# Kernel optimization log

Hardware: AMD Instinct MI355X
Metric: run time of the kernel (lower is better)

## Reference

```python
import jax, jax.numpy as jnp
import numpy as np

KSIZE = 7       # patch size
STRIDE_Q = 4    # stride_1: query patch stride
STRIDE_KV = 1   # stride_2: key/value patch stride
SCALE = 10.0    # softmax_scale


def unfold(x, k, stride, pad):
    """torch.nn.Unfold equivalent. x:[B,C,H,W] -> [B, C*k*k, L] (c-major, then kh, kw)."""
    x = jnp.pad(x, ((0, 0), (0, 0), (pad, pad), (pad, pad)))
    B, C, Hp, Wp = x.shape
    nh = (Hp - k) // stride + 1
    nw = (Wp - k) // stride + 1
    sl = lambda i, n: slice(i, i + (n - 1) * stride + 1, stride)
    # [B, C, k*k, nh, nw]
    pat = jnp.stack([x[:, :, sl(i, nh), sl(j, nw)] for i in range(k) for j in range(k)], axis=2)
    return pat.reshape(B, C * k * k, nh * nw)


def fold(p, k, stride, pad, H, W):
    """torch.nn.functional.fold equivalent (overlap-add). p:[B, C*k*k, L] -> [B,C,H,W]."""
    B, D, L = p.shape
    C = D // (k * k)
    nh = (H + 2 * pad - k) // stride + 1
    nw = (W + 2 * pad - k) // stride + 1
    p = p.reshape(B, C, k, k, nh, nw)
    out = jnp.zeros((B, C, H + 2 * pad, W + 2 * pad), p.dtype)
    sl = lambda i, n: slice(i, i + (n - 1) * stride + 1, stride)
    for i in range(k):
        for j in range(k):
            out = out.at[:, :, sl(i, nh), sl(j, nw)].add(p[:, :, i, j])
    return out[:, :, pad:pad + H, pad:pad + W]


def conv1x1(x, w, bias):
    # w: [out, in]
    return jnp.einsum('bihw,oi->bohw', x, w) + bias[None, :, None, None]


def setup_inputs() -> dict:
    key = jax.random.key(0)
    ks = jax.random.split(key, 9)
    B, Cin, H, W = 4, 64, 128, 128
    Cit = 16
    s_in = 1.0 / np.sqrt(Cin)
    s_it = 1.0 / np.sqrt(Cit)
    return {
        'b': jax.random.normal(ks[0], (B, Cin, H, W), jnp.float32),
        'g_w': jax.random.normal(ks[1], (Cit, Cin), jnp.float32) * s_in,
        'g_b': jax.random.normal(ks[2], (Cit,), jnp.float32) * 0.01,
        'th_w': jax.random.normal(ks[3], (Cit, Cin), jnp.float32) * s_in,
        'th_b': jax.random.normal(ks[4], (Cit,), jnp.float32) * 0.01,
        'ph_w': jax.random.normal(ks[5], (Cit, Cin), jnp.float32) * s_in,
        'ph_b': jax.random.normal(ks[6], (Cit,), jnp.float32) * 0.01,
        'o_w': jax.random.normal(ks[7], (Cin, Cit), jnp.float32) * s_it,
        'o_b': jax.random.normal(ks[8], (Cin,), jnp.float32) * 0.01,
    }


def reference(b, g_w, g_b, th_w, th_b, ph_w, ph_b, o_w, o_b):
    B, Cin, H, W = b.shape
    pad = KSIZE // 2
    b1 = conv1x1(b, g_w, g_b)      # queries source  [B,16,H,W]
    b2 = conv1x1(b, th_w, th_b)    # values source
    b3 = conv1x1(b, ph_w, ph_b)    # keys source

    Q = unfold(b1, KSIZE, STRIDE_Q, pad).transpose(0, 2, 1)   # [B, L1, D]
    K = unfold(b3, KSIZE, STRIDE_KV, pad).transpose(0, 2, 1)  # [B, L2, D]
    V = unfold(b2, KSIZE, STRIDE_KV, pad).transpose(0, 2, 1)  # [B, L2, D]

    scores = jnp.einsum('bqd,bkd->bqk', Q, K)                 # [B, L1, L2]
    attn = jax.nn.softmax(scores * SCALE, axis=-1)
    Zp = jnp.einsum('bqk,bkd->bqd', attn, V).transpose(0, 2, 1)  # [B, D, L1]

    y = fold(Zp, KSIZE, STRIDE_Q, pad, H, W)                  # overlap-add
    Zc = fold(jnp.ones_like(Zp), KSIZE, STRIDE_Q, pad, H, W)  # overlap counts
    y = y / Zc
    y = conv1x1(y, o_w, o_b)
    return b + y
```

## Files before the change

### kernel.cpp

```cpp
#include <hip/hip_runtime.h>
#include <math.h>

#define NB 4
#define CIN 64
#define CIT 16
#define KS 7
#define PAD 3
#define HH 128
#define WW 128
#define HP 134
#define WPS 136
#define L1 1024
#define DD 784
#define SCALE_F 10.0f
#define WSCR 3.5f
#define TCAP 128
#define WEPS 1e-7f

#define NPIX (HP * WPS)
#define NHWCF (NB * NPIX * CIT)
#define RSTR 2176
#define WROW 352

typedef __attribute__((ext_vector_type(4))) float f32x4;
typedef __attribute__((ext_vector_type(8))) short s16x8;
typedef __attribute__((ext_vector_type(4))) unsigned int u32x4;

__device__ __forceinline__ unsigned short f2bf(float f) {
    unsigned u = __float_as_uint(f);
    unsigned r = (u + 0x7FFFu + ((u >> 16) & 1u)) >> 16;
    return (unsigned short)r;
}

__global__ __launch_bounds__(256) void k_prep(
    const float* __restrict__ bin,
    const float* __restrict__ gw, const float* __restrict__ gb,
    const float* __restrict__ tw, const float* __restrict__ tb,
    const float* __restrict__ pw, const float* __restrict__ pb,
    float* __restrict__ b1f, float* __restrict__ b2f, float* __restrict__ b3f,
    unsigned short* __restrict__ b1n, unsigned short* __restrict__ b3n)
{
    int p = blockIdx.x * 256 + threadIdx.x;
    if (p >= NB * NPIX) return;
    int x = p % WPS; int r = p / WPS; int y = r % HP; int bb = r / HP;
    bool inter = (x >= PAD && x < PAD + WW && y >= PAD && y < PAD + HH);
    float v[CIN];
    if (inter) {
        int iy = y - PAD, ix = x - PAD;
        const float* src = bin + ((size_t)(bb * CIN) * HH + iy) * WW + ix;
        #pragma unroll
        for (int ci = 0; ci < CIN; ++ci) v[ci] = src[ci * HH * WW];
    }
    float a1v[CIT], a2v[CIT], a3v[CIT];
    unsigned short o1[CIT], o3[CIT];
    #pragma unroll
    for (int co = 0; co < CIT; ++co) {
        float a1 = 0.f, a2 = 0.f, a3 = 0.f;
        if (inter) {
            a1 = gb[co]; a2 = tb[co]; a3 = pb[co];
            #pragma unroll
            for (int ci = 0; ci < CIN; ++ci) {
                float vv = v[ci];
                a1 += gw[co * CIN + ci] * vv;
                a2 += tw[co * CIN + ci] * vv;
                a3 += pw[co * CIN + ci] * vv;
            }
        }
        a1v[co] = a1; a2v[co] = a2; a3v[co] = a3;
        o1[co] = f2bf(a1); o3[co] = f2bf(a3);
    }
    size_t pb16 = (size_t)p * CIT;
    #pragma unroll
    for (int g = 0; g < 4; ++g) {
        f32x4 w1 = {a1v[4*g], a1v[4*g+1], a1v[4*g+2], a1v[4*g+3]};
        f32x4 w2 = {a2v[4*g], a2v[4*g+1], a2v[4*g+2], a2v[4*g+3]};
        f32x4 w3 = {a3v[4*g], a3v[4*g+1], a3v[4*g+2], a3v[4*g+3]};
        *(f32x4*)(b1f + pb16 + 4*g) = w1;
        *(f32x4*)(b2f + pb16 + 4*g) = w2;
        *(f32x4*)(b3f + pb16 + 4*g) = w3;
    }
    unsigned pk1[8], pk3[8];
    #pragma unroll
    for (int kk = 0; kk < 8; ++kk) {
        pk1[kk] = (unsigned)o1[2 * kk] | ((unsigned)o1[2 * kk + 1] << 16);
        pk3[kk] = (unsigned)o3[2 * kk] | ((unsigned)o3[2 * kk + 1] << 16);
    }
    unsigned short* d1 = b1n + pb16;
    unsigned short* d3 = b3n + pb16;
    u32x4 w1a = {pk1[0], pk1[1], pk1[2], pk1[3]}, w1b = {pk1[4], pk1[5], pk1[6], pk1[7]};
    u32x4 w3a = {pk3[0], pk3[1], pk3[2], pk3[3]}, w3b = {pk3[4], pk3[5], pk3[6], pk3[7]};
    *(u32x4*)d1 = w1a; *(u32x4*)(d1 + 8) = w1b;
    *(u32x4*)d3 = w3a; *(u32x4*)(d3 + 8) = w3b;
}

__global__ __launch_bounds__(512, 2) void k_screen(
    const unsigned short* __restrict__ b1n, const unsigned short* __restrict__ b3n,
    _Float16* __restrict__ tmaxh)
{
    int blk = blockIdx.x;
    int qt = blk & 3;
    int qh = (blk >> 2) & 31;
    int bb = blk >> 7;
    int qstart_ky = qt * 32;
    int tid = threadIdx.x;
    int lane = tid & 63, w = tid >> 6;
    int lanelow = lane & 15;
    int h = (lane >> 5) & 1;
    int clo = (lane >> 4) & 1;

    __shared__ __align__(16) short smem[16 * RSTR];

    const unsigned short* b1nb = b1n + (size_t)bb * (NPIX * CIT);
    const unsigned short* b3nb = b3n + (size_t)bb * (NPIX * CIT);

    int qybase = 4 * qh;
    size_t qb0 = ((size_t)((bb * 64 + 2 * qh) * 16 + lanelow)) * 1024 + qt * 256 + w;
    size_t qb1 = ((size_t)((bb * 64 + 2 * qh + 1) * 16 + lanelow)) * 1024 + qt * 256 + w;

    for (int task = tid; task < 1600; task += 512) {
        int pp = task % 50, qq = task / 50;
        u32x4 lo = {0, 0, 0, 0}, hi = {0, 0, 0, 0};
        if (pp < 49) {
            int i = pp / 7, j = pp % 7;
            int qx = 4 * qq;
            const unsigned short* src = b1nb + ((size_t)(qybase + i) * WPS + qx + j) * CIT;
            lo = *(const u32x4*)src; hi = *(const u32x4*)(src + 8);
        }
        short* dst = smem + (qq * 50 + pp) * 16;
        *(u32x4*)dst = lo; *(u32x4*)(dst + 8) = hi;
    }
    __syncthreads();

    s16x8 B0[25], B1[25];
    #pragma unroll
    for (int s = 0; s < 25; ++s) {
        int ko = s * 32 + ((lane >> 4) & 3) * 8;
        B0[s] = *(const s16x8*)(smem + lanelow * 800 + ko);
        B1[s] = *(const s16x8*)(smem + (lanelow + 16) * 800 + ko);
    }
    __syncthreads();

    short* kring = smem;
    for (int task = tid; task < 16 * 272; task += 512) {
        int rr = task / 272, ch = task % 272;
        *(u32x4*)(kring + rr * RSTR + ch * 8) =
            *(const u32x4*)(b3nb + (size_t)(qstart_ky + rr) * (WPS * CIT) + ch * 8);
    }
    __syncthreads();

    int abase = (w * 16 + lanelow) * 16 + clo * 8;

    for (int p = 0; p < 4; ++p) {
        __builtin_amdgcn_s_setprio(1);
        for (int it8 = 0; it8 < 8; ++it8) {
            int it = 8 * p + it8;
            int ky = qstart_ky + it;
            f32x4 C0 = {0.f, 0.f, 0.f, 0.f}, C1 = {0.f, 0.f, 0.f, 0.f};
            #pragma unroll
            for (int s = 0; s < 25; ++s) {
                const int pe = 2 * s;
                const int po = (2 * s + 1 < 49) ? (2 * s + 1) : 0;
                const int ie = pe / 7, je = pe % 7;
                const int io = po / 7, jo = po % 7;
                int i_h = h ? io : ie;
                int j_h = h ? jo : je;
                int slot = (ky + i_h) & 15;
                const short* ap = kring + slot * RSTR + j_h * 16 + abase;
                s16x8 a0 = *(const s16x8*)ap;
                C0 = __builtin_amdgcn_mfma_f32_16x16x32_bf16(a0, B0[s], C0, 0, 0, 0);
                C1 = __builtin_amdgcn_mfma_f32_16x16x32_bf16(a0, B1[s], C1, 0, 0, 0);
            }
            float lm0 = fmaxf(fmaxf(C0[0], C0[1]), fmaxf(C0[2], C0[3]));
            lm0 = fmaxf(lm0, __shfl_xor(lm0, 16));
            lm0 = fmaxf(lm0, __shfl_xor(lm0, 32));
            float lm1 = fmaxf(fmaxf(C1[0], C1[1]), fmaxf(C1[2], C1[3]));
            lm1 = fmaxf(lm1, __shfl_xor(lm1, 16));
            lm1 = fmaxf(lm1, __shfl_xor(lm1, 32));
            if (lane < 16) {
                tmaxh[qb0 + it * 8] = (_Float16)lm0;
                tmaxh[qb1 + it * 8] = (_Float16)lm1;
            }
        }
        __builtin_amdgcn_s_setprio(0);
        __syncthreads();
        if (p < 3) {
            int rbase = qstart_ky + 8 * p + 16;
            for (int task = tid; task < 8 * 272; task += 512) {
                int rr = task / 272, ch = task % 272;
                int row = rbase + rr;
                int srow = (row < HP) ? row : (HP - 1);
                *(u32x4*)(kring + (row & 15) * RSTR + ch * 8) =
                    *(const u32x4*)(b3nb + (size_t)srow * (WPS * CIT) + ch * 8);
            }
            __syncthreads();
        }
    }
}

__global__ __launch_bounds__(256) void k_finalize(
    const float* __restrict__ b1f, const float* __restrict__ b2f,
    const float* __restrict__ b3f, const _Float16* __restrict__ tmaxh,
    float* __restrict__ Zp)
{
    int wv = threadIdx.x >> 6;
    int lane = threadIdx.x & 63;
    int gq = blockIdx.x * 4 + wv;
    int bb = gq >> 10, q = gq & 1023;
    int qh = q >> 5, qw = q & 31;
    int qy = qh * 4, qx = qw * 4;
    int ch = lane & 15, pbase = lane >> 4;

    __shared__ int tq[4][TCAP];
    __shared__ __align__(16) float wbufs[4][7 * WROW];

    const float* b1b = b1f + (size_t)bb * (NPIX * CIT);
    const float* b2b = b2f + (size_t)bb * (NPIX * CIT);
    const float* b3b = b3f + (size_t)bb * (NPIX * CIT);

    const _Float16* qb = tmaxh + ((size_t)((bb * 64 + (q >> 4)) * 16 + (q & 15))) * 1024;
    _Float16 tvh[16];
    *(u32x4*)&tvh[0] = *(const u32x4*)(qb + (size_t)lane * 16);
    *(u32x4*)&tvh[8] = *(const u32x4*)(qb + (size_t)lane * 16 + 8);
    float tv[16]; float mg = -1e30f;
    #pragma unroll
    for (int k = 0; k < 16; ++k) {
        tv[k] = (float)tvh[k];
        mg = fmaxf(mg, tv[k]);
    }
    #pragma unroll
    for (int o = 32; o > 0; o >>= 1) mg = fmaxf(mg, __shfl_xor(mg, o));
    float thr = mg - WSCR;

    int cnt = 0;
    #pragma unroll
    for (int k = 0; k < 16; ++k) {
        bool p = (tv[k] >= thr);
        unsigned long long mk = __ballot(p);
        if (p) {
            int pos = cnt + (int)__popcll(mk & ((1ull << lane) - 1ull));
            if (pos < TCAP) tq[wv][pos] = lane * 16 + k;
        }
        cnt += (int)__popcll(mk);
    }
    int nt = min(cnt, TCAP);
    __syncthreads();

    int wrow[10], wxf[10]; bool wok[10];
    #pragma unroll
    for (int t = 0; t < 10; ++t) {
        int task = lane + 64 * t;
        wok[t] = (task < 616);
        wrow[t] = (task < 616) ? (task / 88) : 0;
        wxf[t] = (task < 616) ? ((task % 88) * 4) : 0;
    }

    float qreg[13]; int offs[13]; int loff[13];
    int qorg = (qy * WPS + qx) * CIT;
    #pragma unroll
    for (int k = 0; k < 13; ++k) {
        int p = pbase + 4 * k;
        if (p < 49) {
            int pi = p / 7, pj = p % 7;
            offs[k] = (pi * WPS + pj) * CIT + ch;
            loff[k] = pi * WROW + pj * CIT + ch;
            qreg[k] = b1b[qorg + offs[k]];
        } else { offs[k] = 0; loff[k] = 0; qreg[k] = 0.f; }
    }
    float* wbuf = wbufs[wv];

    float m = -1e30f, l = 0.f, acc[13];
    #pragma unroll
    for (int k = 0; k < 13; ++k) acc[k] = 0.f;

    f32x4 pf[10];
    if (nt > 0) {
        int e0 = tq[wv][0];
        const float* ws0 = b3b + (size_t)((e0 >> 3) * WPS + (e0 & 7) * 16) * CIT;
        #pragma unroll
        for (int t = 0; t < 10; ++t)
            if (wok[t]) pf[t] = *(const f32x4*)(ws0 + (size_t)wrow[t] * (WPS * CIT) + wxf[t]);
    }

    for (int ti = 0; ti < nt; ++ti) {
        int e = tq[wv][ti];
        int ky = e >> 3;
        int kxb = (e & 7) * 16;
        #pragma unroll
        for (int t = 0; t < 10; ++t)
            if (wok[t]) *(f32x4*)(wbuf + wrow[t] * WROW + wxf[t]) = pf[t];
        if (ti + 1 < nt) {
            int e2 = tq[wv][ti + 1];
            const float* ws2 = b3b + (size_t)((e2 >> 3) * WPS + (e2 & 7) * 16) * CIT;
            #pragma unroll
            for (int t = 0; t < 10; ++t)
                if (wok[t]) pf[t] = *(const f32x4*)(ws2 + (size_t)wrow[t] * (WPS * CIT) + wxf[t]);
        }
        for (int c4 = 0; c4 < 4; ++c4) {
            float kvv[4][13];
            #pragma unroll
            for (int u = 0; u < 4; ++u) {
                int cib = (c4 * 4 + u) * CIT;
                #pragma unroll
                for (int k = 0; k < 13; ++k) kvv[u][k] = wbuf[loff[k] + cib];
            }
            float s[4];
            #pragma unroll
            for (int u = 0; u < 4; ++u) {
                float t = 0.f;
                #pragma unroll
                for (int k = 0; k < 13; ++k) t += qreg[k] * kvv[u][k];
                #pragma unroll
                for (int o = 32; o > 0; o >>= 1) t += __shfl_xor(t, o);
                s[u] = t;
            }
            float mnew = fmaxf(m, fmaxf(fmaxf(s[0], s[1]), fmaxf(s[2], s[3])));
            float sc = __expf(SCALE_F * (m - mnew));
            float wk[4];
            wk[0] = __expf(SCALE_F * (s[0] - mnew));
            wk[1] = __expf(SCALE_F * (s[1] - mnew));
            wk[2] = __expf(SCALE_F * (s[2] - mnew));
            wk[3] = __expf(SCALE_F * (s[3] - mnew));
            l = l * sc + (wk[0] + wk[1] + wk[2] + wk[3]);
            m = mnew;
            float wmx = fmaxf(fmaxf(wk[0], wk[1]), fmaxf(wk[2], wk[3]));
            if (wmx > WEPS) {
                #pragma unroll
                for (int k = 0; k < 13; ++k) acc[k] *= sc;
                #pragma unroll
                for (int u = 0; u < 4; ++u) {
                    if (wk[u] > WEPS) {
                        int kb = (ky * WPS + kxb + c4 * 4 + u) * CIT;
                        #pragma unroll
                        for (int k = 0; k < 13; ++k) acc[k] += wk[u] * b2b[kb + offs[k]];
                    }
                }
            }
        }
    }

    float inv = (nt > 0) ? (1.f / l) : 0.f;
    float* zq = Zp + (size_t)gq * DD;
    #pragma unroll
    for (int k = 0; k < 13; ++k) {
        int d = lane + 64 * k;
        if (d < DD) zq[d] = acc[k] * inv;
    }
}

__global__ __launch_bounds__(256) void k_fold(
    const float* __restrict__ bin, const float* __restrict__ ow,
    const float* __restrict__ ob, const float* __restrict__ Zp,
    float* __restrict__ outp)
{
    int p = blockIdx.x * 256 + threadIdx.x;
    if (p >= NB * HH * WW) return;
    int ox = p % WW; int r = p / WW; int oy = r % HH; int bb = r / HH;
    int yp = oy + PAD, xp = ox + PAD;
    int qh0 = (yp - 3) >> 2, qh1 = min(31, yp >> 2);
    int qw0 = (xp - 3) >> 2, qw1 = min(31, xp >> 2);
    float cnt = (float)((qh1 - qh0 + 1) * (qw1 - qw0 + 1));
    float y16[CIT];
    #pragma unroll
    for (int c = 0; c < CIT; ++c) y16[c] = 0.f;
    for (int qhh = qh0; qhh <= qh1; ++qhh) {
        int i = yp - 4 * qhh;
        for (int qww = qw0; qww <= qw1; ++qww) {
            int j = xp - 4 * qww;
            const float* zb = Zp + (size_t)((bb << 10) + qhh * 32 + qww) * DD + (i * 7 + j) * CIT;
            #pragma unroll
            for (int c = 0; c < CIT; ++c) y16[c] += zb[c];
        }
    }
    float icnt = 1.f / cnt;
    #pragma unroll
    for (int c = 0; c < CIT; ++c) y16[c] *= icnt;
    size_t oidx = ((size_t)(bb * CIN) * HH + oy) * WW + ox;
    for (int co = 0; co < CIN; ++co) {
        float a = ob[co];
        #pragma unroll
        for (int c = 0; c < CIT; ++c) a += ow[co * CIT + c] * y16[c];
        outp[oidx + (size_t)co * HH * WW] = bin[oidx + (size_t)co * HH * WW] + a;
    }
}

extern "C" void kernel_launch(void* const* d_in, const int* in_sizes, int n_in,
                              void* d_out, int out_size, void* d_ws, size_t ws_size,
                              hipStream_t stream) {
    (void)in_sizes; (void)n_in; (void)out_size; (void)ws_size;
    const float* bin = (const float*)d_in[0];
    const float* gw  = (const float*)d_in[1];
    const float* gb  = (const float*)d_in[2];
    const float* tw  = (const float*)d_in[3];
    const float* tb  = (const float*)d_in[4];
    const float* pw  = (const float*)d_in[5];
    const float* pb  = (const float*)d_in[6];
    const float* ow  = (const float*)d_in[7];
    const float* ob  = (const float*)d_in[8];

    float* outp = (float*)d_out;
    float* b3f = outp;
    float* b1f = outp + NHWCF;
    unsigned short* b3n = (unsigned short*)(outp + 2 * (size_t)NHWCF);
    unsigned short* b1n = b3n + NHWCF;

    float* ws = (float*)d_ws;
    float* b2f = ws;
    float* Zp  = ws + NHWCF;
    _Float16* tmaxh = (_Float16*)(ws + NHWCF + (size_t)NB * L1 * DD);

    hipLaunchKernelGGL(k_prep, dim3((NB * NPIX + 255) / 256), dim3(256), 0, stream,
                       bin, gw, gb, tw, tb, pw, pb, b1f, b2f, b3f, b1n, b3n);
    hipLaunchKernelGGL(k_screen, dim3(512), dim3(512), 0, stream,
                       b1n, b3n, tmaxh);
    hipLaunchKernelGGL(k_finalize, dim3(1024), dim3(256), 0, stream,
                       b1f, b2f, b3f, tmaxh, Zp);
    hipLaunchKernelGGL(k_fold, dim3((NB * HH * WW + 255) / 256), dim3(256), 0, stream,
                       bin, ow, ob, Zp, outp);
}
```

Before: 215.7 us.

## Process four query rows per screen block to reuse key ring loads

Each k_screen block now handles four query rows instead of two, holding four sets of B fragments in registers and issuing four MFMAs per key fragment load. The grid is halved from 512 to 256 blocks. The aim is to halve the key-ring staging traffic and LDS reads per MFMA. The cost is many more VGPRs (100 extra s16x8 vectors), which risks spills or lower occupancy under launch_bounds(512,2), and fewer blocks to spread across CUs.

```diff
diff --git a/kernel.cpp b/kernel.cpp
--- a/kernel.cpp
+++ b/kernel.cpp
@@ -99,8 +99,8 @@
 {
     int blk = blockIdx.x;
     int qt = blk & 3;
-    int qh = (blk >> 2) & 31;
-    int bb = blk >> 7;
+    int qhp = (blk >> 2) & 15;
+    int bb = blk >> 6;
     int qstart_ky = qt * 32;
     int tid = threadIdx.x;
     int lane = tid & 63, w = tid >> 6;
@@ -113,32 +113,60 @@
     const unsigned short* b1nb = b1n + (size_t)bb * (NPIX * CIT);
     const unsigned short* b3nb = b3n + (size_t)bb * (NPIX * CIT);
 
-    int qybase = 4 * qh;
-    size_t qb0 = ((size_t)((bb * 64 + 2 * qh) * 16 + lanelow)) * 1024 + qt * 256 + w;
-    size_t qb1 = ((size_t)((bb * 64 + 2 * qh + 1) * 16 + lanelow)) * 1024 + qt * 256 + w;
-
-    for (int task = tid; task < 1600; task += 512) {
-        int pp = task % 50, qq = task / 50;
-        u32x4 lo = {0, 0, 0, 0}, hi = {0, 0, 0, 0};
-        if (pp < 49) {
-            int i = pp / 7, j = pp % 7;
-            int qx = 4 * qq;
-            const unsigned short* src = b1nb + ((size_t)(qybase + i) * WPS + qx + j) * CIT;
-            lo = *(const u32x4*)src; hi = *(const u32x4*)(src + 8);
-        }
-        short* dst = smem + (qq * 50 + pp) * 16;
-        *(u32x4*)dst = lo; *(u32x4*)(dst + 8) = hi;
-    }
-    __syncthreads();
-
-    s16x8 B0[25], B1[25];
-    #pragma unroll
-    for (int s = 0; s < 25; ++s) {
-        int ko = s * 32 + ((lane >> 4) & 3) * 8;
-        B0[s] = *(const s16x8*)(smem + lanelow * 800 + ko);
-        B1[s] = *(const s16x8*)(smem + (lanelow + 16) * 800 + ko);
-    }
-    __syncthreads();
+    size_t qb0 = ((size_t)((bb * 64 + 4 * qhp + 0) * 16 + lanelow)) * 1024 + qt * 256 + w;
+    size_t qb1 = ((size_t)((bb * 64 + 4 * qhp + 1) * 16 + lanelow)) * 1024 + qt * 256 + w;
+    size_t qb2 = ((size_t)((bb * 64 + 4 * qhp + 2) * 16 + lanelow)) * 1024 + qt * 256 + w;
+    size_t qb3 = ((size_t)((bb * 64 + 4 * qhp + 3) * 16 + lanelow)) * 1024 + qt * 256 + w;
+
+    s16x8 B0[25], B1[25], B2[25], B3[25];
+    int koff = ((lane >> 4) & 3) * 8;
+
+    {
+        int qybase = 8 * qhp;
+        for (int task = tid; task < 1600; task += 512) {
+            int pp = task % 50, qq = task / 50;
+            u32x4 lo = {0, 0, 0, 0}, hi = {0, 0, 0, 0};
+            if (pp < 49) {
+                int i = pp / 7, j = pp % 7;
+                int qx = 4 * qq;
+                const unsigned short* src = b1nb + ((size_t)(qybase + i) * WPS + qx + j) * CIT;
+                lo = *(const u32x4*)src; hi = *(const u32x4*)(src + 8);
+            }
+            short* dst = smem + (qq * 50 + pp) * 16;
+            *(u32x4*)dst = lo; *(u32x4*)(dst + 8) = hi;
+        }
+        __syncthreads();
+        #pragma unroll
+        for (int s = 0; s < 25; ++s) {
+            int ko = s * 32 + koff;
+            B0[s] = *(const s16x8*)(smem + lanelow * 800 + ko);
+            B1[s] = *(const s16x8*)(smem + (lanelow + 16) * 800 + ko);
+        }
+        __syncthreads();
+    }
+    {
+        int qybase = 8 * qhp + 4;
+        for (int task = tid; task < 1600; task += 512) {
+            int pp = task % 50, qq = task / 50;
+            u32x4 lo = {0, 0, 0, 0}, hi = {0, 0, 0, 0};
+            if (pp < 49) {
+                int i = pp / 7, j = pp % 7;
+                int qx = 4 * qq;
+                const unsigned short* src = b1nb + ((size_t)(qybase + i) * WPS + qx + j) * CIT;
+                lo = *(const u32x4*)src; hi = *(const u32x4*)(src + 8);
+            }
+            short* dst = smem + (qq * 50 + pp) * 16;
+            *(u32x4*)dst = lo; *(u32x4*)(dst + 8) = hi;
+        }
+        __syncthreads();
+        #pragma unroll
+        for (int s = 0; s < 25; ++s) {
+            int ko = s * 32 + koff;
+            B2[s] = *(const s16x8*)(smem + lanelow * 800 + ko);
+            B3[s] = *(const s16x8*)(smem + (lanelow + 16) * 800 + ko);
+        }
+        __syncthreads();
+    }
 
     short* kring = smem;
     for (int task = tid; task < 16 * 272; task += 512) {
@@ -156,6 +184,7 @@
             int it = 8 * p + it8;
             int ky = qstart_ky + it;
             f32x4 C0 = {0.f, 0.f, 0.f, 0.f}, C1 = {0.f, 0.f, 0.f, 0.f};
+            f32x4 C2 = {0.f, 0.f, 0.f, 0.f}, C3 = {0.f, 0.f, 0.f, 0.f};
             #pragma unroll
             for (int s = 0; s < 25; ++s) {
                 const int pe = 2 * s;
@@ -169,6 +198,8 @@
                 s16x8 a0 = *(const s16x8*)ap;
                 C0 = __builtin_amdgcn_mfma_f32_16x16x32_bf16(a0, B0[s], C0, 0, 0, 0);
                 C1 = __builtin_amdgcn_mfma_f32_16x16x32_bf16(a0, B1[s], C1, 0, 0, 0);
+                C2 = __builtin_amdgcn_mfma_f32_16x16x32_bf16(a0, B2[s], C2, 0, 0, 0);
+                C3 = __builtin_amdgcn_mfma_f32_16x16x32_bf16(a0, B3[s], C3, 0, 0, 0);
             }
             float lm0 = fmaxf(fmaxf(C0[0], C0[1]), fmaxf(C0[2], C0[3]));
             lm0 = fmaxf(lm0, __shfl_xor(lm0, 16));
@@ -176,9 +207,17 @@
             float lm1 = fmaxf(fmaxf(C1[0], C1[1]), fmaxf(C1[2], C1[3]));
             lm1 = fmaxf(lm1, __shfl_xor(lm1, 16));
             lm1 = fmaxf(lm1, __shfl_xor(lm1, 32));
+            float lm2 = fmaxf(fmaxf(C2[0], C2[1]), fmaxf(C2[2], C2[3]));
+            lm2 = fmaxf(lm2, __shfl_xor(lm2, 16));
+            lm2 = fmaxf(lm2, __shfl_xor(lm2, 32));
+            float lm3 = fmaxf(fmaxf(C3[0], C3[1]), fmaxf(C3[2], C3[3]));
+            lm3 = fmaxf(lm3, __shfl_xor(lm3, 16));
+            lm3 = fmaxf(lm3, __shfl_xor(lm3, 32));
             if (lane < 16) {
                 tmaxh[qb0 + it * 8] = (_Float16)lm0;
                 tmaxh[qb1 + it * 8] = (_Float16)lm1;
+                tmaxh[qb2 + it * 8] = (_Float16)lm2;
+                tmaxh[qb3 + it * 8] = (_Float16)lm3;
             }
         }
         __builtin_amdgcn_s_setprio(0);
@@ -410,7 +449,7 @@
 
     hipLaunchKernelGGL(k_prep, dim3((NB * NPIX + 255) / 256), dim3(256), 0, stream,
                        bin, gw, gb, tw, tb, pw, pb, b1f, b2f, b3f, b1n, b3n);
-    hipLaunchKernelGGL(k_screen, dim3(512), dim3(512), 0, stream,
+    hipLaunchKernelGGL(k_screen, dim3(256), dim3(512), 0, stream,
                        b1n, b3n, tmaxh);
     hipLaunchKernelGGL(k_finalize, dim3(1024), dim3(256), 0, stream,
                        b1f, b2f, b3f, tmaxh, Zp);
```

Measured after the change: 713.4 us. +230.7%, slower.
